# Performance work log

Hardware: AMD Instinct MI355X
Metric: run time of the kernel (lower is better)

The kernel has to match this reference:

```python
import jax, jax.numpy as jnp
import numpy as np


def setup_inputs() -> dict:
    key = jax.random.key(0)
    n_clusters, dim_latent = 16, 64
    batch, L = 512, 10
    # upper-triangular pair indices (A, B) as in LatentSpace.__init__
    A_np, B_np = np.nonzero(np.triu(np.ones((n_clusters, n_clusters))))
    n_states = A_np.shape[0]  # 136
    k1, k2 = jax.random.split(key)
    z = jax.random.normal(k1, (batch, L, dim_latent), dtype=jnp.float32)
    mu = jax.random.uniform(k2, (dim_latent, n_clusters), dtype=jnp.float32,
                            minval=-1.0, maxval=1.0)
    pi = jnp.ones((1, n_states), jnp.float32) / n_states
    return {
        "z": z,
        "mu": mu,
        "pi": pi,
        "A": jnp.asarray(A_np, jnp.int32),
        "B": jnp.asarray(B_np, jnp.int32),
    }


def reference(z, mu, pi, A, B):
    """Faithful port of LatentSpace.call(z, inference=False) -> log_p_z (scalar)."""
    LOG2PI = jnp.log(jnp.asarray(2.0 * np.pi, jnp.float32))
    d = z.shape[-1]

    mu_A = mu[:, A]            # [d, S]
    mu_B = mu[:, B]            # [d, S]
    a1 = mu_B - mu_A           # [d, S]
    a2 = z[..., None] - mu_B[None, None]          # [b, L, d, S]

    inv_sig = jnp.sum(a1 * a1, axis=0)            # [S]
    # tf.math.reciprocal_no_nan: 0 where inv_sig == 0
    safe = jnp.where(inv_sig == 0, 1.0, inv_sig)
    recip = jnp.where(inv_sig == 0, 0.0, 1.0 / safe)

    _mu = -jnp.einsum('ds,blds->bls', a1, a2) * recip   # [b, L, S]
    sq_a2 = jnp.sum(a2 * a2, axis=2)                     # [b, L, S]
    _t = -sq_a2 + _mu ** 2 * inv_sig

    sd = jnp.sqrt(inv_sig + 1e-12)
    cdf = jax.scipy.special.ndtr  # gradient is the normal pdf, same as custom_gradient
    log_p_z_c_L = (0.5 * (LOG2PI - jnp.log(inv_sig + 1e-12) + _t)
                   + jnp.log(cdf((1.0 - _mu) * sd) - cdf(-_mu * sd) + 1e-12))

    log_pi = jnp.log(jax.nn.softmax(pi, axis=-1) + 1e-12)   # [1, S]
    log_p_zc_L = (-0.5 * d * LOG2PI
                  + log_pi[:, None, :]
                  + jnp.where(inv_sig == 0, -0.5 * sq_a2, log_p_z_c_L))  # [b, L, S]

    log_p_z_L = jax.scipy.special.logsumexp(log_p_zc_L, axis=-1, keepdims=True)
    log_p_z = jnp.mean(log_p_z_L)
    return log_p_z
```

## Files before the change

### kernel.cpp

```cpp
#include <hip/hip_runtime.h>
#include <math.h>

#define LOG2PI 1.8378770664093453f
#define NSTATES 136
#define NROWS 5120
#define DIM 64
#define NCLUST 16

__device__ __forceinline__ float ndtrf(float x) {
    return 0.5f * erfcf(-x * 0.70710678118654752f);
}

__global__ __launch_bounds__(256) void state_consts_kernel(
    const float* __restrict__ mu,
    const float* __restrict__ pi,
    const int* __restrict__ A, const int* __restrict__ B,
    float4* __restrict__ k0, float4* __restrict__ k1)
{
    __shared__ float musm[DIM * NCLUST];
    __shared__ float pis[NSTATES];
    __shared__ float sm_m, sm_z;
    int tid = threadIdx.x;
    for (int i = tid; i < DIM * NCLUST; i += 256) musm[i] = mu[i];
    if (tid < NSTATES) pis[tid] = pi[tid];
    __syncthreads();
    if (tid == 0) {
        float m = -1e30f;
        for (int s = 0; s < NSTATES; ++s) m = fmaxf(m, pis[s]);
        float zz = 0.f;
        for (int s = 0; s < NSTATES; ++s) zz += expf(pis[s] - m);
        sm_m = m; sm_z = zz;
    }
    __syncthreads();
    if (tid < NSTATES) {
        int a = A[tid], b = B[tid];
        float c1 = 0.f, nb2 = 0.f, iv = 0.f;
        for (int d = 0; d < DIM; ++d) {
            float mA = musm[d * NCLUST + a];
            float mB = musm[d * NCLUST + b];
            float a1 = mB - mA;
            c1  += a1 * mB;
            nb2 += mB * mB;
            iv  += a1 * a1;
        }
        float recip  = (iv == 0.f) ? 0.f : 1.f / iv;
        float sd     = sqrtf(iv + 1e-12f);
        float loginv = logf(iv + 1e-12f);
        float lp     = logf(expf(pis[tid] - sm_m) / sm_z + 1e-12f);
        float lcomb  = lp - 31.5f * LOG2PI - 0.5f * loginv;
        float lzero  = lp - 32.0f * LOG2PI;
        k0[tid] = make_float4(c1, nb2, recip, sd);
        k1[tid] = make_float4(lcomb, lzero, 0.f, 0.f);
    }
}

__global__ __launch_bounds__(256) void latent_main_kernel(
    const float* __restrict__ z,
    const float* __restrict__ mu,
    const int* __restrict__ A, const int* __restrict__ B,
    const float4* __restrict__ k0g, const float4* __restrict__ k1g,
    float* __restrict__ out)
{
    __shared__ float muT[NCLUST][68];
    __shared__ float4 k0s[NSTATES];
    __shared__ float4 k1s[NSTATES];
    __shared__ int2  abs_[NSTATES];
    __shared__ float redbuf[4];

    int tid = threadIdx.x;
    for (int i = tid; i < DIM * NCLUST; i += 256) {
        int d = i >> 4, c = i & 15;
        muT[c][d] = mu[i];
    }
    if (tid < NSTATES) {
        k0s[tid] = k0g[tid];
        k1s[tid] = k1g[tid];
        abs_[tid] = make_int2(A[tid], B[tid]);
    }
    __syncthreads();

    int w = tid >> 6, lane = tid & 63;
    int chunk = lane >> 4, c = lane & 15;
    int gw = blockIdx.x * 4 + w;

    float acc = 0.f;
    #pragma unroll
    for (int rr = 0; rr < 2; ++rr) {
        int r = gw * 2 + rr;

        const float4* zp = (const float4*)(z + (size_t)r * DIM + chunk * 16);
        const float4* mp = (const float4*)(&muT[c][chunk * 16]);
        float dotc = 0.f, zn = 0.f;
        #pragma unroll
        for (int i = 0; i < 4; ++i) {
            float4 z4 = zp[i];
            float4 m4 = mp[i];
            dotc += z4.x * m4.x + z4.y * m4.y + z4.z * m4.z + z4.w * m4.w;
            zn   += z4.x * z4.x + z4.y * z4.y + z4.z * z4.z + z4.w * z4.w;
        }
        dotc += __shfl_xor(dotc, 16);
        dotc += __shfl_xor(dotc, 32);
        zn   += __shfl_xor(zn, 16);
        zn   += __shfl_xor(zn, 32);

        float vmax = -INFINITY;
        float vals[3];
        #pragma unroll
        for (int it = 0; it < 3; ++it) {
            int s = it * 64 + lane;
            bool valid = (s < NSTATES);
            int ss = valid ? s : 0;
            int2 ab = abs_[ss];
            float4 K0 = k0s[ss];
            float4 K1 = k1s[ss];
            float cza = __shfl(dotc, ab.x);
            float czb = __shfl(dotc, ab.y);
            float dot = czb - cza - K0.x;
            float sq  = zn - 2.f * czb + K0.y;
            float mu_ = -dot * K0.z;
            float t   = -sq + dot * dot * K0.z;
            float dcdf = ndtrf((1.f - mu_) * K0.w) - ndtrf(-mu_ * K0.w);
            float v_n = K1.x + 0.5f * t + logf(dcdf + 1e-12f);
            float v_z = K1.y - 0.5f * sq;
            float v = (K0.z == 0.f) ? v_z : v_n;
            if (!valid) v = -INFINITY;
            vals[it] = v;
            vmax = fmaxf(vmax, v);
        }
        #pragma unroll
        for (int m = 1; m < 64; m <<= 1) vmax = fmaxf(vmax, __shfl_xor(vmax, m));
        float se = expf(vals[0] - vmax) + expf(vals[1] - vmax) + expf(vals[2] - vmax);
        #pragma unroll
        for (int m = 1; m < 64; m <<= 1) se += __shfl_xor(se, m);
        acc += vmax + logf(se);
    }

    if (lane == 0) redbuf[w] = acc;
    __syncthreads();
    if (tid == 0) {
        float t = redbuf[0] + redbuf[1] + redbuf[2] + redbuf[3];
        atomicAdd(out, t * (1.0f / (float)NROWS));
    }
}

extern "C" void kernel_launch(void* const* d_in, const int* in_sizes, int n_in,
                              void* d_out, int out_size, void* d_ws, size_t ws_size,
                              hipStream_t stream) {
    const float* z  = (const float*)d_in[0];
    const float* mu = (const float*)d_in[1];
    const float* pi = (const float*)d_in[2];
    const int*   A  = (const int*)d_in[3];
    const int*   B  = (const int*)d_in[4];
    float* out = (float*)d_out;

    float4* k0 = (float4*)d_ws;
    float4* k1 = k0 + NSTATES;

    hipMemsetAsync(d_out, 0, sizeof(float), stream);
    state_consts_kernel<<<1, 256, 0, stream>>>(mu, pi, A, B, k0, k1);
    latent_main_kernel<<<640, 256, 0, stream>>>(z, mu, A, B, k0, k1, out);
}
```

Baseline: 84.03 us.

## Fold output zeroing into setup kernel, parallelize softmax, use online logsumexp

Removes the separate memset launch by zeroing the output inside the state-constants kernel. The single-thread softmax reduction over pi becomes a wave-level shuffle reduction. The per-row logsumexp switches from two shuffle passes (max, then sum) to one online max/sum pass, which adds extra exps per shuffle step. Invalid lanes now use a large negative constant instead of -inf so the online merge avoids inf-minus-inf NaNs.

```diff
diff --git a/kernel.cpp b/kernel.cpp
--- a/kernel.cpp
+++ b/kernel.cpp
@@ -6,6 +6,7 @@
 #define NROWS 5120
 #define DIM 64
 #define NCLUST 16
+#define NEG_BIG -1e30f
 
 __device__ __forceinline__ float ndtrf(float x) {
     return 0.5f * erfcf(-x * 0.70710678118654752f);
@@ -15,21 +16,27 @@
     const float* __restrict__ mu,
     const float* __restrict__ pi,
     const int* __restrict__ A, const int* __restrict__ B,
-    float4* __restrict__ k0, float4* __restrict__ k1)
+    float4* __restrict__ k0, float4* __restrict__ k1,
+    float* __restrict__ out)
 {
     __shared__ float musm[DIM * NCLUST];
     __shared__ float pis[NSTATES];
     __shared__ float sm_m, sm_z;
     int tid = threadIdx.x;
+    if (tid == 0) out[0] = 0.f;
     for (int i = tid; i < DIM * NCLUST; i += 256) musm[i] = mu[i];
     if (tid < NSTATES) pis[tid] = pi[tid];
     __syncthreads();
-    if (tid == 0) {
-        float m = -1e30f;
-        for (int s = 0; s < NSTATES; ++s) m = fmaxf(m, pis[s]);
-        float zz = 0.f;
-        for (int s = 0; s < NSTATES; ++s) zz += expf(pis[s] - m);
-        sm_m = m; sm_z = zz;
+    if (tid < 64) {
+        float m = NEG_BIG;
+        for (int i = tid; i < NSTATES; i += 64) m = fmaxf(m, pis[i]);
+        #pragma unroll
+        for (int d = 1; d < 64; d <<= 1) m = fmaxf(m, __shfl_xor(m, d));
+        float s = 0.f;
+        for (int i = tid; i < NSTATES; i += 64) s += expf(pis[i] - m);
+        #pragma unroll
+        for (int d = 1; d < 64; d <<= 1) s += __shfl_xor(s, d);
+        if (tid == 0) { sm_m = m; sm_z = s; }
     }
     __syncthreads();
     if (tid < NSTATES) {
@@ -103,7 +110,6 @@
         zn   += __shfl_xor(zn, 16);
         zn   += __shfl_xor(zn, 32);
 
-        float vmax = -INFINITY;
         float vals[3];
         #pragma unroll
         for (int it = 0; it < 3; ++it) {
@@ -123,16 +129,20 @@
             float v_n = K1.x + 0.5f * t + logf(dcdf + 1e-12f);
             float v_z = K1.y - 0.5f * sq;
             float v = (K0.z == 0.f) ? v_z : v_n;
-            if (!valid) v = -INFINITY;
-            vals[it] = v;
-            vmax = fmaxf(vmax, v);
+            vals[it] = valid ? v : NEG_BIG;
         }
+
+        float m = fmaxf(fmaxf(vals[0], vals[1]), vals[2]);
+        float s = expf(vals[0] - m) + expf(vals[1] - m) + expf(vals[2] - m);
         #pragma unroll
-        for (int m = 1; m < 64; m <<= 1) vmax = fmaxf(vmax, __shfl_xor(vmax, m));
-        float se = expf(vals[0] - vmax) + expf(vals[1] - vmax) + expf(vals[2] - vmax);
-        #pragma unroll
-        for (int m = 1; m < 64; m <<= 1) se += __shfl_xor(se, m);
-        acc += vmax + logf(se);
+        for (int d = 1; d < 64; d <<= 1) {
+            float mo = __shfl_xor(m, d);
+            float so = __shfl_xor(s, d);
+            float mn = fmaxf(m, mo);
+            s = s * expf(m - mn) + so * expf(mo - mn);
+            m = mn;
+        }
+        acc += m + logf(s);
     }
 
     if (lane == 0) redbuf[w] = acc;
@@ -156,7 +166,6 @@
     float4* k0 = (float4*)d_ws;
     float4* k1 = k0 + NSTATES;
 
-    hipMemsetAsync(d_out, 0, sizeof(float), stream);
-    state_consts_kernel<<<1, 256, 0, stream>>>(mu, pi, A, B, k0, k1);
+    state_consts_kernel<<<1, 256, 0, stream>>>(mu, pi, A, B, k0, k1, out);
     latent_main_kernel<<<640, 256, 0, stream>>>(z, mu, A, B, k0, k1, out);
 }
```

New measurement: 79.25 us. 1.06x faster.
